# Performance work log

Measured on AMD Instinct MI355X. Metric: run time of the kernel, lower is better.

## Reference

```python
import jax, jax.numpy as jnp
import numpy as np

CHUNK = 32
HEADS = 4
EPS_RMS = 1e-5

def silu(x):
    return jax.nn.silu(x)

def l2norm(x, eps=1e-6):
    return x * jax.lax.rsqrt(jnp.sum(x * x, axis=-1, keepdims=True) + eps)

def short_conv(x, w):
    # x: (b, l, c); w: (c, K) depthwise causal conv, no bias
    K = w.shape[1]
    L = x.shape[1]
    xp = jnp.pad(x, ((0, 0), (K - 1, 0), (0, 0)))
    out = xp[:, 0:L, :] * w[:, 0]
    for k in range(1, K):
        out = out + xp[:, k:k + L, :] * w[:, k]
    return out

def delta_rule_chunkwise(q, k, v, beta, chunk=CHUNK):
    # q,k: (b,h,l,dk); v: (b,h,l,dv); beta: (b,h,l). l divisible by chunk.
    b, h, l, dk = q.shape
    dv = v.shape[-1]
    n = l // chunk
    q = l2norm(q)
    k = l2norm(k)
    v = v * beta[..., None]
    k_beta = k * beta[..., None]
    resh = lambda x: x.reshape(b, h, n, chunk, -1)
    q, k, v, k_beta = map(resh, (q, k, v, k_beta))
    strict_lower = jnp.tril(jnp.ones((chunk, chunk), bool), -1)
    # A = -(k_beta k^T) kept strictly lower triangular
    attn = jnp.where(strict_lower, -(k_beta @ jnp.swapaxes(k, -1, -2)), 0.0)
    # forward substitution: T = (I - A)^{-1} - I built row by row (fixed 32 rows)
    for i in range(1, chunk):
        row = attn[..., i, :]                                  # (b,h,n,c)
        new = attn[..., i, :i] + jnp.einsum('...j,...jk->...k', row, attn[..., :, :i])
        attn = attn.at[..., i, :i].set(new)
    attn = attn + jnp.eye(chunk, dtype=attn.dtype)
    u = attn @ v        # (b,h,n,c,dv)
    w = attn @ k_beta   # (b,h,n,c,dk)
    lower_incl = jnp.tril(jnp.ones((chunk, chunk), bool))
    qc, kc, uc, wc = [jnp.moveaxis(x, 2, 0) for x in (q, k, u, w)]
    S0 = jnp.zeros((b, h, dk, dv), q.dtype)
    def step(S, inp):
        q_i, k_i, u_i, w_i = inp
        attn_i = jnp.where(lower_incl, q_i @ jnp.swapaxes(k_i, -1, -2), 0.0)
        u_adj = u_i - w_i @ S
        o_i = q_i @ S + attn_i @ u_adj
        S = S + jnp.swapaxes(k_i, -1, -2) @ u_adj
        return S, o_i
    S, o = jax.lax.scan(step, S0, (qc, kc, uc, wc))
    o = jnp.moveaxis(o, 0, 2).reshape(b, h, l, dv)
    return o, S

def ema_rule(v, gamma):
    # v: (b,h,l,dv), gamma: (b,h,l); sequential EMA scan
    v_t = jnp.moveaxis(v, 2, 0)       # (l,b,h,dv)
    g_t = jnp.moveaxis(gamma, 2, 0)   # (l,b,h)
    s0 = jnp.zeros(v.shape[:2] + (v.shape[-1],), v.dtype)
    def step(s, inp):
        vt, gt = inp
        s = gt[..., None] * s + (1.0 - gt[..., None]) * vt
        return s, s
    s_fin, out = jax.lax.scan(step, s0, (v_t, g_t))
    return jnp.moveaxis(out, 0, 2), s_fin

def rms_norm(x, w, eps=EPS_RMS):
    return x * jax.lax.rsqrt(jnp.mean(x * x, axis=-1, keepdims=True) + eps) * w

def setup_inputs() -> dict:
    key = jax.random.key(0)
    ks = jax.random.split(key, 16)
    b, l, d = 4, 2048, 1024
    H, conv_K = HEADS, 4
    s = 0.02
    return {
        'hidden_states': jax.random.normal(ks[0], (b, l, d), jnp.float32),
        'Wq': jax.random.normal(ks[1], (d, d), jnp.float32) * s,
        'Wk': jax.random.normal(ks[2], (d, d), jnp.float32) * s,
        'Wv': jax.random.normal(ks[3], (d, d), jnp.float32) * s,
        'conv_q': jax.random.normal(ks[4], (d, conv_K), jnp.float32) * 0.3,
        'conv_k': jax.random.normal(ks[5], (d, conv_K), jnp.float32) * 0.3,
        'conv_v': jax.random.normal(ks[6], (d, conv_K), jnp.float32) * 0.3,
        'Wb': jax.random.normal(ks[7], (d, H), jnp.float32) * s,
        'Wdec': jax.random.normal(ks[8], (d, H), jnp.float32) * s,
        'Wmix': jax.random.normal(ks[9], (d, H), jnp.float32) * s,
        'conv_mix': jax.random.normal(ks[10], (H, conv_K), jnp.float32) * 0.3,
        'mix_bias': jnp.full((H,), -2.0, jnp.float32),
        'rms_w': jnp.ones((d // H,), jnp.float32),
        'Wo': jax.random.normal(ks[11], (d, d), jnp.float32) * s,
    }

def reference(hidden_states, Wq, Wk, Wv, conv_q, conv_k, conv_v, Wb, Wdec, Wmix, conv_mix, mix_bias, rms_w, Wo):
    b, l, d = hidden_states.shape
    H = HEADS
    dk = d // H
    dv = d // H
    # projections + causal depthwise short conv (silu activation inside conv)
    q = silu(short_conv(hidden_states @ Wq, conv_q))
    k = silu(short_conv(hidden_states @ Wk, conv_k))
    v = silu(short_conv(hidden_states @ Wv, conv_v))
    mix_inp = silu(short_conv(hidden_states @ Wmix, conv_mix))  # (b,l,H)
    # qk_activation == 'silu' applies an extra silu after conv (per source)
    q = silu(q)
    k = silu(k)
    # split heads -> (b,H,l,dh)
    to_heads = lambda x, dh: jnp.transpose(x.reshape(b, l, H, dh), (0, 2, 1, 3))
    q_d = to_heads(q, dk)
    k_d = to_heads(k, dk)
    v_d = to_heads(v, dv)
    beta = jax.nn.sigmoid(hidden_states @ Wb)           # (b,l,H)
    beta_d = jnp.transpose(beta, (0, 2, 1))             # (b,H,l)
    o_d, S = delta_rule_chunkwise(q_d, k_d, v_d, beta_d)
    o_d = jnp.transpose(o_d, (0, 2, 1, 3))              # (b,l,H,dv)
    # EMA branch
    gamma = jax.nn.sigmoid(hidden_states @ Wdec)        # (b,l,H)
    gamma_d = jnp.transpose(gamma, (0, 2, 1))
    ema_out, ema_state = ema_rule(v_d, gamma_d)
    ema_out = jnp.transpose(ema_out, (0, 2, 1, 3))      # (b,l,H,dv)
    # fine-grained head mix gate
    mix = jax.nn.sigmoid(mix_inp + mix_bias)            # (b,l,H)
    o = (1.0 - mix[..., None]) * o_d + mix[..., None] * ema_out
    # per-head RMSNorm then output projection
    o = rms_norm(o, rms_w)
    out = o.reshape(b, l, H * dv) @ Wo
    return out
```

## Files before the change

kernel.cpp:

```cpp
#include <hip/hip_runtime.h>
#include <hip/hip_bf16.h>

#define B 4
#define L 2048
#define D 1024
#define NH 4
#define DK 256
#define CHUNK 32
#define NCH 64
#define BH (B*NH)
#define ET 64
#define ENCH (L/ET)
#define TB 16

typedef __attribute__((ext_vector_type(8))) __bf16 bf16x8;
typedef __attribute__((ext_vector_type(4))) __bf16 bf16x4;
typedef __attribute__((ext_vector_type(4))) float f32x4;

__device__ inline unsigned short f2bf(float f) {
    union { float f; unsigned u; } v; v.f = f;
    unsigned r = v.u + 0x7fffu + ((v.u >> 16) & 1u);
    return (unsigned short)(r >> 16);
}
__device__ inline float bf2f(unsigned short h) {
    union { unsigned u; float f; } v; v.u = ((unsigned)h) << 16; return v.f;
}
__device__ inline float sigmoidf_(float x) { return 1.0f / (1.0f + __expf(-x)); }
__device__ inline float siluf_(float x) { return x / (1.0f + __expf(-x)); }

#define MFMA16(a, b, c) __builtin_amdgcn_mfma_f32_16x16x32_bf16((a), (b), (c), 0, 0, 0)

__device__ inline void bar_lds() {
    __builtin_amdgcn_s_waitcnt(0xC07F);
    __builtin_amdgcn_s_barrier();
}

__device__ inline void load_lds16(const unsigned short* g, unsigned short* l) {
    __builtin_amdgcn_global_load_lds(
        (const __attribute__((address_space(1))) unsigned int*)g,
        (__attribute__((address_space(3))) unsigned int*)l, 16, 0, 0);
}

__global__ __launch_bounds__(256) void k_wT(const float* Wq, const float* Wk, const float* Wv,
                                            const float* Wo, unsigned short* wT)
{
    __shared__ float tile[32][33];
    int z = blockIdx.z;
    const float* W = (z == 0) ? Wq : (z == 1) ? Wk : (z == 2) ? Wv : Wo;
    unsigned short* out = wT + (size_t)z * D * D;
    int kt = blockIdx.x * 32, nt = blockIdx.y * 32;
    int tx = threadIdx.x & 31, ty = threadIdx.x >> 5;
#pragma unroll
    for (int i = 0; i < 4; i++)
        tile[ty + 8 * i][tx] = W[(size_t)(kt + ty + 8 * i) * D + nt + tx];
    __syncthreads();
#pragma unroll
    for (int i = 0; i < 4; i++)
        out[(size_t)(nt + ty + 8 * i) * D + kt + tx] = f2bf(tile[tx][ty + 8 * i]);
}

__global__ __launch_bounds__(256) void k_cvt(const float* h, unsigned short* hb, int n4)
{
    int i = blockIdx.x * blockDim.x + threadIdx.x;
    int stride = gridDim.x * blockDim.x;
    const float4* h4 = (const float4*)h;
    for (; i < n4; i += stride) {
        float4 v = h4[i];
        ushort4 o;
        o.x = f2bf(v.x); o.y = f2bf(v.y); o.z = f2bf(v.z); o.w = f2bf(v.w);
        *(ushort4*)(hb + 4 * (size_t)i) = o;
    }
}

template<int NTOT, bool OUT_F32>
__global__ __launch_bounds__(256) void k_gemm_lds(const unsigned short* __restrict__ A,
                                                  const unsigned short* __restrict__ BT,
                                                  void* __restrict__ outp)
{
    __shared__ __align__(16) unsigned short As[128 * 32];
    __shared__ __align__(16) unsigned short Bs[128 * 32];
    const int K = 1024;
    int tid = threadIdx.x;
    int w = tid >> 6, lane = tid & 63;
    int r16 = lane & 15, quad = lane >> 4;
    int wm = w & 1, wn = w >> 1;
    int bm = blockIdx.x * 128;
    int bn = blockIdx.y * 128;
    int lrow = lane >> 2;
    int lcol = (lane & 3) * 8;
    f32x4 z4 = {0.f, 0.f, 0.f, 0.f};
    f32x4 acc[4][4];
#pragma unroll
    for (int i = 0; i < 4; i++)
#pragma unroll
        for (int j = 0; j < 4; j++) acc[i][j] = z4;

    for (int kt = 0; kt < K; kt += 32) {
#pragma unroll
        for (int j = 0; j < 2; j++) {
            int r0 = (w * 2 + j) * 16;
            load_lds16(A + (size_t)(bm + r0 + lrow) * K + kt + lcol, &As[r0 * 32]);
            load_lds16(BT + (size_t)(bn + r0 + lrow) * K + kt + lcol, &Bs[r0 * 32]);
        }
        __syncthreads();
        bf16x8 af[4], bf[4];
#pragma unroll
        for (int ms = 0; ms < 4; ms++)
            af[ms] = *(const bf16x8*)&As[(wm * 64 + ms * 16 + r16) * 32 + quad * 8];
#pragma unroll
        for (int ns = 0; ns < 4; ns++)
            bf[ns] = *(const bf16x8*)&Bs[(wn * 64 + ns * 16 + r16) * 32 + quad * 8];
#pragma unroll
        for (int ms = 0; ms < 4; ms++)
#pragma unroll
            for (int ns = 0; ns < 4; ns++)
                acc[ms][ns] = MFMA16(af[ms], bf[ns], acc[ms][ns]);
        __syncthreads();
    }
#pragma unroll
    for (int ms = 0; ms < 4; ms++)
#pragma unroll
        for (int ns = 0; ns < 4; ns++)
#pragma unroll
            for (int r = 0; r < 4; r++) {
                int m = bm + wm * 64 + ms * 16 + quad * 4 + r;
                int n = bn + wn * 64 + ns * 16 + r16;
                if (OUT_F32)
                    ((float*)outp)[(size_t)m * NTOT + n] = acc[ms][ns][r];
                else
                    ((unsigned short*)outp)[(size_t)m * NTOT + n] = f2bf(acc[ms][ns][r]);
            }
}

__global__ __launch_bounds__(256) void k_smallproj(const float* hid, const float* Wb, const float* Wd,
                                                   const float* Wm, float* beta, float* gamma, float* xmix)
{
    int wave = threadIdx.x >> 6, lane = threadIdx.x & 63;
    int row = blockIdx.x * 4 + wave;
    const float* hrow = hid + (size_t)row * D;
    float acc[12];
#pragma unroll
    for (int j = 0; j < 12; j++) acc[j] = 0.f;
    for (int i = 0; i < 16; i++) {
        int k = lane + 64 * i;
        float h = hrow[k];
        float4 wb = ((const float4*)Wb)[k];
        float4 wd = ((const float4*)Wd)[k];
        float4 wm = ((const float4*)Wm)[k];
        acc[0] += h * wb.x; acc[1] += h * wb.y; acc[2] += h * wb.z; acc[3] += h * wb.w;
        acc[4] += h * wd.x; acc[5] += h * wd.y; acc[6] += h * wd.z; acc[7] += h * wd.w;
        acc[8] += h * wm.x; acc[9] += h * wm.y; acc[10] += h * wm.z; acc[11] += h * wm.w;
    }
#pragma unroll
    for (int j = 0; j < 12; j++)
        for (int off = 32; off; off >>= 1) acc[j] += __shfl_xor(acc[j], off, 64);
    if (lane < 4) {
        beta[(size_t)row * 4 + lane] = sigmoidf_(acc[lane]);
        gamma[(size_t)row * 4 + lane] = sigmoidf_(acc[4 + lane]);
        xmix[(size_t)row * 4 + lane] = acc[8 + lane];
    }
}

__global__ __launch_bounds__(256) void k_convnorm(const unsigned short* __restrict__ xqkv,
                                                  const float* __restrict__ cq,
                                                  const float* __restrict__ ck,
                                                  const float* __restrict__ cv,
                                                  unsigned short* __restrict__ qn,
                                                  unsigned short* __restrict__ kn,
                                                  unsigned short* __restrict__ vb)
{
    int blk = blockIdx.x;
    int b = blk >> 7;
    int t0 = (blk & 127) * TB;
    int tid = threadIdx.x;
    int h = tid >> 6, lane = tid & 63;
    int c = tid * 4;

    float wq[4][4], wk[4][4], wv[4][4];
#pragma unroll
    for (int j = 0; j < 4; j++) {
        float4 a = *(const float4*)(cq + (size_t)(c + j) * 4);
        wq[j][0] = a.x; wq[j][1] = a.y; wq[j][2] = a.z; wq[j][3] = a.w;
        float4 d4 = *(const float4*)(ck + (size_t)(c + j) * 4);
        wk[j][0] = d4.x; wk[j][1] = d4.y; wk[j][2] = d4.z; wk[j][3] = d4.w;
        float4 e = *(const float4*)(cv + (size_t)(c + j) * 4);
        wv[j][0] = e.x; wv[j][1] = e.y; wv[j][2] = e.z; wv[j][3] = e.w;
    }

    float aq[4][4], ak[4][4], av[4][4];
#pragma unroll
    for (int s = 0; s < 4; s++)
#pragma unroll
        for (int j = 0; j < 4; j++) { aq[s][j] = 0.f; ak[s][j] = 0.f; av[s][j] = 0.f; }

    const unsigned short* xb = xqkv + (size_t)(b * L) * (3 * D) + c;

#pragma unroll
    for (int p = 0; p < 3; p++) {
        int r = t0 - 3 + p;
        if (r >= 0) {
            const unsigned short* pp = xb + (size_t)r * (3 * D);
            ushort4 xq = *(const ushort4*)pp;
            ushort4 xk = *(const ushort4*)(pp + D);
            ushort4 xv = *(const ushort4*)(pp + 2 * D);
            float fq[4] = {bf2f(xq.x), bf2f(xq.y), bf2f(xq.z), bf2f(xq.w)};
            float fk[4] = {bf2f(xk.x), bf2f(xk.y), bf2f(xk.z), bf2f(xk.w)};
            float fv[4] = {bf2f(xv.x), bf2f(xv.y), bf2f(xv.z), bf2f(xv.w)};
#pragma unroll
            for (int d = 3 - p; d <= 3; d++) {
                int s = (p + d + 1) & 3;
                int kk = 3 - d;
#pragma unroll
                for (int j = 0; j < 4; j++) {
                    aq[s][j] += wq[j][kk] * fq[j];
                    ak[s][j] += wk[j][kk] * fk[j];
                    av[s][j] += wv[j][kk] * fv[j];
                }
            }
        }
    }

    ushort4 sq2[2], sk2[2], sv2[2];
    {
        const unsigned short* pp = xb + (size_t)t0 * (3 * D);
        sq2[0] = *(const ushort4*)pp;
        sk2[0] = *(const ushort4*)(pp + D);
        sv2[0] = *(const ushort4*)(pp + 2 * D);
    }

#pragma unroll
    for (int i = 0; i < TB; i++) {
        if (i + 1 < TB) {
            const unsigned short* pp = xb + (size_t)(t0 + i + 1) * (3 * D);
            sq2[(i + 1) & 1] = *(const ushort4*)pp;
            sk2[(i + 1) & 1] = *(const ushort4*)(pp + D);
            sv2[(i + 1) & 1] = *(const ushort4*)(pp + 2 * D);
        }
        {
            ushort4 xq = sq2[i & 1], xk = sk2[i & 1], xv = sv2[i & 1];
            float fq[4] = {bf2f(xq.x), bf2f(xq.y), bf2f(xq.z), bf2f(xq.w)};
            float fk[4] = {bf2f(xk.x), bf2f(xk.y), bf2f(xk.z), bf2f(xk.w)};
            float fv[4] = {bf2f(xv.x), bf2f(xv.y), bf2f(xv.z), bf2f(xv.w)};
#pragma unroll
            for (int d = 0; d < 4; d++) {
                if (i + d < TB) {
                    int s = (i + d) & 3;
                    int kk = 3 - d;
#pragma unroll
                    for (int j = 0; j < 4; j++) {
                        aq[s][j] += wq[j][kk] * fq[j];
                        ak[s][j] += wk[j][kk] * fk[j];
                        av[s][j] += wv[j][kk] * fv[j];
                    }
                }
            }
        }
        {
            const int s = i & 3;
            float rq[4], rk[4], rv[4];
#pragma unroll
            for (int j = 0; j < 4; j++) {
                rq[j] = siluf_(siluf_(aq[s][j]));
                rk[j] = siluf_(siluf_(ak[s][j]));
                rv[j] = siluf_(av[s][j]);
            }
            float sqs = rq[0] * rq[0] + rq[1] * rq[1] + rq[2] * rq[2] + rq[3] * rq[3];
            float sks = rk[0] * rk[0] + rk[1] * rk[1] + rk[2] * rk[2] + rk[3] * rk[3];
            for (int off = 32; off; off >>= 1) {
                sqs += __shfl_xor(sqs, off, 64);
                sks += __shfl_xor(sks, off, 64);
            }
            float qs = rsqrtf(sqs + 1e-6f), ks = rsqrtf(sks + 1e-6f);
            int t = t0 + i;
            size_t oidx = ((size_t)(b * NH + h) * L + t) * DK + lane * 4;
            ushort4 oq, ok, ov;
            oq.x = f2bf(rq[0] * qs); oq.y = f2bf(rq[1] * qs); oq.z = f2bf(rq[2] * qs); oq.w = f2bf(rq[3] * qs);
            ok.x = f2bf(rk[0] * ks); ok.y = f2bf(rk[1] * ks); ok.z = f2bf(rk[2] * ks); ok.w = f2bf(rk[3] * ks);
            ov.x = f2bf(rv[0]); ov.y = f2bf(rv[1]); ov.z = f2bf(rv[2]); ov.w = f2bf(rv[3]);
            *(ushort4*)(qn + oidx) = oq;
            *(ushort4*)(kn + oidx) = ok;
            *(ushort4*)(vb + (size_t)(b * L + t) * D + c) = ov;
            if (i + 4 < TB) {
#pragma unroll
                for (int j = 0; j < 4; j++) { aq[s][j] = 0.f; ak[s][j] = 0.f; av[s][j] = 0.f; }
            }
        }
    }
}

__global__ __launch_bounds__(256) void k_convmix(const float* xmix, const float* cmix, float* mixinp)
{
    int idx = blockIdx.x * 256 + threadIdx.x;
    int h = idx & 3;
    int t = (idx >> 2) & (L - 1);
    int b = idx >> 13;
    float acc = 0.f;
#pragma unroll
    for (int kk = 0; kk < 4; kk++) {
        int tt = t - 3 + kk;
        if (tt >= 0) acc += cmix[h * 4 + kk] * xmix[((size_t)(b * L + tt) << 2) + h];
    }
    mixinp[idx] = siluf_(acc);
}

#define KTS 40
__global__ __launch_bounds__(256) void k_delta_pre(const unsigned short* qn, const unsigned short* kn,
                                                   const unsigned short* vb, const float* beta,
                                                   unsigned short* wneg, unsigned short* knT,
                                                   unsigned short* attnb, float* u)
{
    __shared__ __align__(16) unsigned short kTl[256 * KTS];
    __shared__ __align__(16) unsigned short vTl[256 * KTS];
    __shared__ __align__(16) unsigned short T2b[32 * KTS];
    __shared__ float Gs[32 * 33];
    int bx = blockIdx.x;
    int bh = bx >> 6, ch = bx & 63;
    int b = bh >> 2, h = bh & 3;
    int t0 = ch * 32;
    int tid = threadIdx.x;
    int w = tid >> 6, lane = tid & 63;
    int r16 = lane & 15, quad = lane >> 4;
    size_t rowbase = (size_t)(bh * L + t0);
    f32x4 z4 = {0.f, 0.f, 0.f, 0.f};

    if (w < 3) {
        int mi = (w == 0) ? 0 : 1;
        int ni = (w == 2) ? 1 : 0;
        const unsigned short* krm = kn + (rowbase + mi * 16 + r16) * DK;
        const unsigned short* krn = kn + (rowbase + ni * 16 + r16) * DK;
        const unsigned short* qrm = qn + (rowbase + mi * 16 + r16) * DK;
        f32x4 g = z4, qk = z4;
#pragma unroll
        for (int kt = 0; kt < 8; kt++) {
            bf16x8 a  = *(const bf16x8*)(krm + kt * 32 + quad * 8);
            bf16x8 bb = *(const bf16x8*)(krn + kt * 32 + quad * 8);
            bf16x8 qa = *(const bf16x8*)(qrm + kt * 32 + quad * 8);
            g  = MFMA16(a, bb, g);
            qk = MFMA16(qa, bb, qk);
        }
#pragma unroll
        for (int r = 0; r < 4; r++) {
            int i = mi * 16 + quad * 4 + r, j = ni * 16 + r16;
            Gs[i * 33 + j] = g[r];
            attnb[(size_t)(bh * 64 + ch) * 1024 + i * 32 + j] =
                (j <= i) ? f2bf(qk[r]) : (unsigned short)0;
        }
    } else {
#pragma unroll
        for (int r = 0; r < 4; r++) {
            int i = quad * 4 + r, j = 16 + r16;
            attnb[(size_t)(bh * 64 + ch) * 1024 + i * 32 + j] = 0;
        }
    }
    {
        int t = tid & 31, c0 = (tid >> 5) * 32;
        const unsigned short* krow = kn + (rowbase + t) * DK + c0;
        const unsigned short* vrow = vb + ((size_t)(b * L + t0 + t)) * D + h * DK + c0;
#pragma unroll
        for (int j = 0; j < 32; j += 4) {
            ushort4 kv = *(const ushort4*)(krow + j);
            ushort4 vv = *(const ushort4*)(vrow + j);
            kTl[(c0 + j + 0) * KTS + t] = kv.x;
            kTl[(c0 + j + 1) * KTS + t] = kv.y;
            kTl[(c0 + j + 2) * KTS + t] = kv.z;
            kTl[(c0 + j + 3) * KTS + t] = kv.w;
            vTl[(c0 + j + 0) * KTS + t] = vv.x;
            vTl[(c0 + j + 1) * KTS + t] = vv.y;
            vTl[(c0 + j + 2) * KTS + t] = vv.z;
            vTl[(c0 + j + 3) * KTS + t] = vv.w;
        }
    }
    __syncthreads();

    if (w == 0) {
        int c = lane & 31;
        float rr[32];
#pragma unroll
        for (int j = 0; j < 32; j++) rr[j] = Gs[j * 33 + c];
        rr[0] = 0.f;
        float bc = beta[(size_t)(b * L + t0 + c) * NH + h];
#pragma unroll
        for (int i = 1; i < 32; i++) {
            float bi = __shfl(bc, i, 64);
            float s = -bi * rr[i];
#pragma unroll
            for (int j = 1; j < i; j++) {
                float aij = -bi * __shfl(rr[i], j, 64);
                s += aij * ((c < j) ? rr[j] : 0.f);
            }
            rr[i] = (c < i) ? s : 0.f;
        }
        if (lane < 32) {
#pragma unroll
            for (int i = 0; i < 32; i++) {
                float val = (rr[i] + ((i == c) ? 1.f : 0.f)) * bc;
                T2b[i * KTS + c] = f2bf(val);
            }
        }
    } else {
        int idx = tid - 64;
        for (int rowc = idx; rowc < 256; rowc += 192) {
            unsigned short* kT = knT + ((size_t)(bh * 64 + ch) * DK + rowc) * 32;
#pragma unroll
            for (int seg = 0; seg < 4; seg++) {
                uint4 d = *(const uint4*)&kTl[rowc * KTS + seg * 8];
                *(uint4*)(kT + seg * 8) = d;
            }
        }
    }
    __syncthreads();

#pragma unroll
    for (int mt = 0; mt < 2; mt++) {
        bf16x8 ta = *(const bf16x8*)&T2b[(mt * 16 + r16) * KTS + quad * 8];
#pragma unroll
        for (int nt2 = 0; nt2 < 4; nt2++) {
            int nt = w * 4 + nt2;
            bf16x8 vb2 = *(const bf16x8*)&vTl[(nt * 16 + r16) * KTS + quad * 8];
            bf16x8 kb = *(const bf16x8*)&kTl[(nt * 16 + r16) * KTS + quad * 8];
            f32x4 uu = MFMA16(ta, vb2, z4);
            f32x4 ww = MFMA16(ta, kb, z4);
            float* ug = u + (rowbase + mt * 16 + quad * 4) * DK + nt * 16 + r16;
            unsigned short* wg = wneg + (rowbase + mt * 16 + quad * 4) * DK + nt * 16 + r16;
#pragma unroll
            for (int r = 0; r < 4; r++) {
                ug[(size_t)r * DK] = uu[r];
                wg[(size_t)r * DK] = f2bf(-ww[r]);
            }
        }
    }
}

__global__ __launch_bounds__(256) void k_ema_local(const unsigned short* v, const float* gamma,
                                                   float* ema_local, float* Acum,
                                                   float* s_end, float* Pchunk)
{
    __shared__ float gsh[ET];
    int blk = blockIdx.x;
    int bh = blk >> 5;
    int ch = blk & (ENCH - 1);
    int b = bh >> 2, h = bh & 3;
    int c = threadIdx.x;
    int t0 = ch * ET;
    if (c < ET) gsh[c] = gamma[(size_t)(b * L + t0 + c) * NH + h];
    __syncthreads();
    const unsigned short* vg = v + (size_t)(b * L + t0) * D + h * DK + c;
    float* eg = ema_local + (size_t)(b * L + t0) * D + h * DK + c;
    float* Ag = Acum + (size_t)bh * L + t0;
    float s = 0.f;
    float A = 1.f;
#pragma unroll 8
    for (int i = 0; i < ET; i++) {
        float g = gsh[i];
        s = g * s + (1.f - g) * bf2f(vg[(size_t)i * D]);
        A *= g;
        eg[(size_t)i * D] = s;
        if (c == 0) Ag[i] = A;
    }
    s_end[((size_t)bh * ENCH + ch) * DK + c] = s;
    if (c == 0) Pchunk[(size_t)bh * ENCH + ch] = A;
}

__global__ __launch_bounds__(256) void k_ema_carry(const float* s_end, const float* Pchunk, float* S_in)
{
    int bh = blockIdx.x;
    int c = threadIdx.x;
    float S = 0.f;
    for (int ch = 0; ch < ENCH; ch++) {
        S_in[((size_t)bh * ENCH + ch) * DK + c] = S;
        float P = Pchunk[(size_t)bh * ENCH + ch];
        S = P * S + s_end[((size_t)bh * ENCH + ch) * DK + c];
    }
}

#define STS 280
#define USTR 40
__global__ __launch_bounds__(128, 1) void k_scan(const unsigned short* qn, const unsigned short* wneg,
                                                 const unsigned short* knT, const unsigned short* attnb,
                                                 const float* u, float* od)
{
    __shared__ __align__(16) unsigned short st[16 * STS];
    __shared__ __align__(16) unsigned short uat[16 * USTR];
    int bh = blockIdx.x;
    int tile = blockIdx.y;
    int b = bh >> 2, h = bh & 3;
    int mo = threadIdx.x >> 6, lane = threadIdx.x & 63;
    int r16 = lane & 15, quad = lane >> 4;
    int cbase = tile * 16;
    f32x4 z4 = {0.f, 0.f, 0.f, 0.f};
    f32x4 sacc[8];
#pragma unroll
    for (int a = 0; a < 8; a++) sacc[a] = z4;
    const unsigned short* qb = qn + (size_t)bh * L * DK;
    const unsigned short* wb = wneg + (size_t)bh * L * DK;
    const float* ub = u + (size_t)bh * L * DK;
    const unsigned short* kTbase = knT + (size_t)bh * 64 * DK * 32;
    const unsigned short* atbase = attnb + (size_t)bh * 64 * 1024;
    int dkb = mo * 128;

    bf16x8 qf[2][8], wf[2][8];
    f32x4 au0[2];

    auto issue = [&](int ch, int par) {
        int t0 = ch * 32;
        const unsigned short* wrow = wb + (size_t)(t0 + 16 * mo + r16) * DK;
        const unsigned short* qrow = qb + (size_t)(t0 + 16 * mo + r16) * DK;
#pragma unroll
        for (int kt = 0; kt < 8; kt++) {
            qf[par][kt] = *(const bf16x8*)(qrow + kt * 32 + quad * 8);
            wf[par][kt] = *(const bf16x8*)(wrow + kt * 32 + quad * 8);
        }
        const float* up = ub + (size_t)(t0 + 16 * mo + quad * 4) * DK + cbase + r16;
        f32x4 a; a[0] = up[0]; a[1] = up[DK]; a[2] = up[2 * DK]; a[3] = up[3 * DK];
        au0[par] = a;
    };

    issue(0, 0);

    auto body = [&](int ch, int par) {
        int t0 = ch * 32;
        bf16x8 af = *(const bf16x8*)(atbase + (size_t)ch * 1024 + (16 * mo + r16) * 32 + quad * 8);
        const unsigned short* kTb = kTbase + (size_t)ch * DK * 32;
        bf16x8 kf[8];
#pragma unroll
        for (int a = 0; a < 8; a++)
            kf[a] = *(const bf16x8*)(kTb + (size_t)(dkb + a * 16 + r16) * 32 + quad * 8);

#pragma unroll
        for (int a = 0; a < 8; a++) {
            uint2 p;
            p.x = f2bf(sacc[a][0]) | ((unsigned)f2bf(sacc[a][1]) << 16);
            p.y = f2bf(sacc[a][2]) | ((unsigned)f2bf(sacc[a][3]) << 16);
            *(uint2*)&st[r16 * STS + dkb + a * 16 + quad * 4] = p;
        }
        if (ch + 1 < NCH) issue(ch + 1, par ^ 1);
        bar_lds();

        f32x4 au = au0[par], ao = z4;
#pragma unroll
        for (int kt = 0; kt < 8; kt++) {
            bf16x8 sfr = *(const bf16x8*)&st[r16 * STS + kt * 32 + quad * 8];
            au = MFMA16(wf[par][kt], sfr, au);
            ao = MFMA16(qf[par][kt], sfr, ao);
        }
        {
            uint2 p;
            p.x = f2bf(au[0]) | ((unsigned)f2bf(au[1]) << 16);
            p.y = f2bf(au[2]) | ((unsigned)f2bf(au[3]) << 16);
            *(uint2*)&uat[r16 * USTR + 16 * mo + quad * 4] = p;
        }
        bar_lds();

        {
            bf16x8 uf = *(const bf16x8*)&uat[r16 * USTR + quad * 8];
            ao = MFMA16(af, uf, ao);
            float* op = od + (size_t)(b * L + t0 + 16 * mo + quad * 4) * D + h * DK + cbase + r16;
            op[0] = ao[0]; op[D] = ao[1]; op[2 * D] = ao[2]; op[3 * D] = ao[3];
#pragma unroll
            for (int a = 0; a < 8; a++)
                sacc[a] = MFMA16(kf[a], uf, sacc[a]);
        }
    };

    for (int ch2 = 0; ch2 < NCH; ch2 += 2) {
        body(ch2, 0);
        body(ch2 + 1, 1);
    }
}

__global__ __launch_bounds__(256) void k_mixrms(const float* od, const float* ema_local,
                                                const float* Acum, const float* S_in,
                                                const float* mixinp,
                                                const float* mix_bias, const float* rms_w,
                                                unsigned short* onorm)
{
    int row = blockIdx.x;
    int tid = threadIdx.x;
    int h = tid >> 6, lane = tid & 63;
    int b = row >> 11, t = row & (L - 1);
    int bh = b * NH + h;
    int ch = t >> 6;
    float m = sigmoidf_(mixinp[(size_t)row * NH + h] + mix_bias[h]);
    int c = tid * 4;
    float A = Acum[(size_t)bh * L + t];
    float4 sin4 = *(const float4*)(S_in + ((size_t)bh * ENCH + ch) * DK + (c & (DK - 1)));
    float4 o = *(const float4*)(od + (size_t)row * D + c);
    float4 e = *(const float4*)(ema_local + (size_t)row * D + c);
    e.x += A * sin4.x; e.y += A * sin4.y; e.z += A * sin4.z; e.w += A * sin4.w;
    float x0 = o.x + m * (e.x - o.x);
    float x1 = o.y + m * (e.y - o.y);
    float x2 = o.z + m * (e.z - o.z);
    float x3 = o.w + m * (e.w - o.w);
    float ss = x0 * x0 + x1 * x1 + x2 * x2 + x3 * x3;
    for (int off = 32; off; off >>= 1) ss += __shfl_xor(ss, off, 64);
    float scale = rsqrtf(ss * (1.0f / 256.0f) + 1e-5f);
    float4 w = *(const float4*)(rms_w + lane * 4);
    uint2 p;
    p.x = f2bf(x0 * scale * w.x) | ((unsigned)f2bf(x1 * scale * w.y) << 16);
    p.y = f2bf(x2 * scale * w.z) | ((unsigned)f2bf(x3 * scale * w.w) << 16);
    *(uint2*)(onorm + (size_t)row * D + c) = p;
}

extern "C" void kernel_launch(void* const* d_in, const int* in_sizes, int n_in,
                              void* d_out, int out_size, void* d_ws, size_t ws_size,
                              hipStream_t stream)
{
    (void)in_sizes; (void)n_in; (void)out_size; (void)ws_size;
    const float* hidden   = (const float*)d_in[0];
    const float* Wq       = (const float*)d_in[1];
    const float* Wk       = (const float*)d_in[2];
    const float* Wv       = (const float*)d_in[3];
    const float* conv_q   = (const float*)d_in[4];
    const float* conv_k   = (const float*)d_in[5];
    const float* conv_v   = (const float*)d_in[6];
    const float* Wb       = (const float*)d_in[7];
    const float* Wdec     = (const float*)d_in[8];
    const float* Wmix     = (const float*)d_in[9];
    const float* conv_mix = (const float*)d_in[10];
    const float* mix_bias = (const float*)d_in[11];
    const float* rms_w    = (const float*)d_in[12];
    const float* Wo       = (const float*)d_in[13];
    float* out = (float*)d_out;

    char* ws = (char*)d_ws;
    size_t off = 0;
    auto alloc = [&](size_t bytes) -> char* {
        char* p = ws + off;
        off += (bytes + 255) & ~(size_t)255;
        return p;
    };
    unsigned short* wT    = (unsigned short*)alloc((size_t)4 * D * D * 2);
    unsigned short* hidB  = (unsigned short*)alloc((size_t)B * L * D * 2);
    unsigned short* xqkv  = (unsigned short*)alloc((size_t)B * L * 3 * D * 2);
    float* beta   = (float*)alloc((size_t)B * L * NH * 4);
    float* gamma  = (float*)alloc((size_t)B * L * NH * 4);
    float* xmix   = (float*)alloc((size_t)B * L * NH * 4);
    float* mixinp = (float*)alloc((size_t)B * L * NH * 4);
    float* qbuf   = (float*)alloc((size_t)B * L * D * 4);
    float* kbuf   = (float*)alloc((size_t)B * L * D * 4);
    unsigned short* vb = (unsigned short*)alloc((size_t)B * L * D * 2);
    float* u      = (float*)alloc((size_t)B * L * D * 4);
    unsigned short* attnb = (unsigned short*)alloc((size_t)BH * NCH * CHUNK * CHUNK * 2);
    unsigned short* onorm = (unsigned short*)alloc((size_t)B * L * D * 2);
    unsigned short* kn    = (unsigned short*)alloc((size_t)B * L * D * 2);
    unsigned short* qn    = (unsigned short*)alloc((size_t)B * L * D * 2);
    float* Acum   = (float*)alloc((size_t)BH * L * 4);
    float* s_end  = (float*)alloc((size_t)BH * ENCH * DK * 4);
    float* Pchunk = (float*)alloc((size_t)BH * ENCH * 4);
    float* S_in   = (float*)alloc((size_t)BH * ENCH * DK * 4);

    unsigned short* wneg = xqkv + (size_t)B * L * D;
    unsigned short* knT  = xqkv + (size_t)2 * B * L * D;
    float* ema_local = qbuf;
    float* od  = kbuf;

    k_wT<<<dim3(32, 32, 4), 256, 0, stream>>>(Wq, Wk, Wv, Wo, wT);
    k_cvt<<<dim3(2048), 256, 0, stream>>>(hidden, hidB, B * L * D / 4);
    k_gemm_lds<3 * D, false><<<dim3(64, 24), 256, 0, stream>>>(hidB, wT, xqkv);
    k_smallproj<<<dim3(B * L / 4), 256, 0, stream>>>(hidden, Wb, Wdec, Wmix, beta, gamma, xmix);
    k_convnorm<<<dim3(B * L / TB), 256, 0, stream>>>(xqkv, conv_q, conv_k, conv_v, qn, kn, vb);
    k_convmix<<<dim3(B * L * NH / 256), 256, 0, stream>>>(xmix, conv_mix, mixinp);
    k_delta_pre<<<dim3(BH * NCH), 256, 0, stream>>>(qn, kn, vb, beta, wneg, knT, attnb, u);
    k_ema_local<<<dim3(BH * ENCH), 256, 0, stream>>>(vb, gamma, ema_local, Acum, s_end, Pchunk);
    k_ema_carry<<<dim3(BH), 256, 0, stream>>>(s_end, Pchunk, S_in);
    k_scan<<<dim3(16, 16), 128, 0, stream>>>(qn, wneg, knT, attnb, u, od);
    k_mixrms<<<dim3(B * L), 256, 0, stream>>>(od, ema_local, Acum, S_in, mixinp, mix_bias, rms_w, onorm);
    k_gemm_lds<D, true><<<dim3(64, 8), 256, 0, stream>>>(onorm, wT + (size_t)3 * D * D, out);
}
```

Baseline: 459.5 us.

## Fuse bf16 conversion into smallproj, remap GEMM tiles per XCD, store intermediates as bf16

Removes the separate hidden-state conversion kernel by having k_smallproj write the bf16 copy while it reads the row, saving one full read of the input. The GEMM block index is remapped so that groups of M-tiles sharing a B column land on the same XCD, which is meant to improve L2 reuse. The delta-rule output and the EMA local output are now stored as bf16 instead of fp32, halving their write and read traffic into the mix/RMS kernel at some cost in precision.

```diff
diff --git a/kernel.cpp b/kernel.cpp
--- a/kernel.cpp
+++ b/kernel.cpp
@@ -59,19 +59,6 @@
         out[(size_t)(nt + ty + 8 * i) * D + kt + tx] = f2bf(tile[tx][ty + 8 * i]);
 }
 
-__global__ __launch_bounds__(256) void k_cvt(const float* h, unsigned short* hb, int n4)
-{
-    int i = blockIdx.x * blockDim.x + threadIdx.x;
-    int stride = gridDim.x * blockDim.x;
-    const float4* h4 = (const float4*)h;
-    for (; i < n4; i += stride) {
-        float4 v = h4[i];
-        ushort4 o;
-        o.x = f2bf(v.x); o.y = f2bf(v.y); o.z = f2bf(v.z); o.w = f2bf(v.w);
-        *(ushort4*)(hb + 4 * (size_t)i) = o;
-    }
-}
-
 template<int NTOT, bool OUT_F32>
 __global__ __launch_bounds__(256) void k_gemm_lds(const unsigned short* __restrict__ A,
                                                   const unsigned short* __restrict__ BT,
@@ -84,8 +71,10 @@
     int w = tid >> 6, lane = tid & 63;
     int r16 = lane & 15, quad = lane >> 4;
     int wm = w & 1, wn = w >> 1;
-    int bm = blockIdx.x * 128;
-    int bn = blockIdx.y * 128;
+    int lin = blockIdx.x + gridDim.x * blockIdx.y;
+    int xcd = lin & 7, tt = lin >> 3;
+    int bm = (xcd * 8 + (tt & 7)) * 128;
+    int bn = (tt >> 3) * 128;
     int lrow = lane >> 2;
     int lcol = (lane & 3) * 8;
     f32x4 z4 = {0.f, 0.f, 0.f, 0.f};
@@ -133,17 +122,20 @@
 }
 
 __global__ __launch_bounds__(256) void k_smallproj(const float* hid, const float* Wb, const float* Wd,
-                                                   const float* Wm, float* beta, float* gamma, float* xmix)
+                                                   const float* Wm, float* beta, float* gamma, float* xmix,
+                                                   unsigned short* hb)
 {
     int wave = threadIdx.x >> 6, lane = threadIdx.x & 63;
     int row = blockIdx.x * 4 + wave;
     const float* hrow = hid + (size_t)row * D;
+    unsigned short* hbrow = hb + (size_t)row * D;
     float acc[12];
 #pragma unroll
     for (int j = 0; j < 12; j++) acc[j] = 0.f;
     for (int i = 0; i < 16; i++) {
         int k = lane + 64 * i;
         float h = hrow[k];
+        hbrow[k] = f2bf(h);
         float4 wb = ((const float4*)Wb)[k];
         float4 wd = ((const float4*)Wd)[k];
         float4 wm = ((const float4*)Wm)[k];
@@ -432,7 +424,7 @@
 }
 
 __global__ __launch_bounds__(256) void k_ema_local(const unsigned short* v, const float* gamma,
-                                                   float* ema_local, float* Acum,
+                                                   unsigned short* ema_local, float* Acum,
                                                    float* s_end, float* Pchunk)
 {
     __shared__ float gsh[ET];
@@ -445,7 +437,7 @@
     if (c < ET) gsh[c] = gamma[(size_t)(b * L + t0 + c) * NH + h];
     __syncthreads();
     const unsigned short* vg = v + (size_t)(b * L + t0) * D + h * DK + c;
-    float* eg = ema_local + (size_t)(b * L + t0) * D + h * DK + c;
+    unsigned short* eg = ema_local + (size_t)(b * L + t0) * D + h * DK + c;
     float* Ag = Acum + (size_t)bh * L + t0;
     float s = 0.f;
     float A = 1.f;
@@ -454,7 +446,7 @@
         float g = gsh[i];
         s = g * s + (1.f - g) * bf2f(vg[(size_t)i * D]);
         A *= g;
-        eg[(size_t)i * D] = s;
+        eg[(size_t)i * D] = f2bf(s);
         if (c == 0) Ag[i] = A;
     }
     s_end[((size_t)bh * ENCH + ch) * DK + c] = s;
@@ -477,7 +469,7 @@
 #define USTR 40
 __global__ __launch_bounds__(128, 1) void k_scan(const unsigned short* qn, const unsigned short* wneg,
                                                  const unsigned short* knT, const unsigned short* attnb,
-                                                 const float* u, float* od)
+                                                 const float* u, unsigned short* od)
 {
     __shared__ __align__(16) unsigned short st[16 * STS];
     __shared__ __align__(16) unsigned short uat[16 * USTR];
@@ -554,8 +546,9 @@
         {
             bf16x8 uf = *(const bf16x8*)&uat[r16 * USTR + quad * 8];
             ao = MFMA16(af, uf, ao);
-            float* op = od + (size_t)(b * L + t0 + 16 * mo + quad * 4) * D + h * DK + cbase + r16;
-            op[0] = ao[0]; op[D] = ao[1]; op[2 * D] = ao[2]; op[3 * D] = ao[3];
+            unsigned short* op = od + (size_t)(b * L + t0 + 16 * mo + quad * 4) * D + h * DK + cbase + r16;
+            op[0] = f2bf(ao[0]); op[D] = f2bf(ao[1]);
+            op[2 * D] = f2bf(ao[2]); op[3 * D] = f2bf(ao[3]);
 #pragma unroll
             for (int a = 0; a < 8; a++)
                 sacc[a] = MFMA16(kf[a], uf, sacc[a]);
@@ -568,7 +561,7 @@
     }
 }
 
-__global__ __launch_bounds__(256) void k_mixrms(const float* od, const float* ema_local,
+__global__ __launch_bounds__(256) void k_mixrms(const unsigned short* od, const unsigned short* ema_local,
                                                 const float* Acum, const float* S_in,
                                                 const float* mixinp,
                                                 const float* mix_bias, const float* rms_w,
@@ -584,13 +577,17 @@
     int c = tid * 4;
     float A = Acum[(size_t)bh * L + t];
     float4 sin4 = *(const float4*)(S_in + ((size_t)bh * ENCH + ch) * DK + (c & (DK - 1)));
-    float4 o = *(const float4*)(od + (size_t)row * D + c);
-    float4 e = *(const float4*)(ema_local + (size_t)row * D + c);
-    e.x += A * sin4.x; e.y += A * sin4.y; e.z += A * sin4.z; e.w += A * sin4.w;
-    float x0 = o.x + m * (e.x - o.x);
-    float x1 = o.y + m * (e.y - o.y);
-    float x2 = o.z + m * (e.z - o.z);
-    float x3 = o.w + m * (e.w - o.w);
+    ushort4 o4 = *(const ushort4*)(od + (size_t)row * D + c);
+    ushort4 e4 = *(const ushort4*)(ema_local + (size_t)row * D + c);
+    float ox = bf2f(o4.x), oy = bf2f(o4.y), oz = bf2f(o4.z), ow = bf2f(o4.w);
+    float ex = bf2f(e4.x) + A * sin4.x;
+    float ey = bf2f(e4.y) + A * sin4.y;
+    float ez = bf2f(e4.z) + A * sin4.z;
+    float ew = bf2f(e4.w) + A * sin4.w;
+    float x0 = ox + m * (ex - ox);
+    float x1 = oy + m * (ey - oy);
+    float x2 = oz + m * (ez - oz);
+    float x3 = ow + m * (ew - ow);
     float ss = x0 * x0 + x1 * x1 + x2 * x2 + x3 * x3;
     for (int off = 32; off; off >>= 1) ss += __shfl_xor(ss, off, 64);
     float scale = rsqrtf(ss * (1.0f / 256.0f) + 1e-5f);
@@ -651,13 +648,12 @@
 
     unsigned short* wneg = xqkv + (size_t)B * L * D;
     unsigned short* knT  = xqkv + (size_t)2 * B * L * D;
-    float* ema_local = qbuf;
-    float* od  = kbuf;
+    unsigned short* ema_local = (unsigned short*)qbuf;
+    unsigned short* od  = (unsigned short*)kbuf;
 
     k_wT<<<dim3(32, 32, 4), 256, 0, stream>>>(Wq, Wk, Wv, Wo, wT);
-    k_cvt<<<dim3(2048), 256, 0, stream>>>(hidden, hidB, B * L * D / 4);
+    k_smallproj<<<dim3(B * L / 4), 256, 0, stream>>>(hidden, Wb, Wdec, Wmix, beta, gamma, xmix, hidB);
     k_gemm_lds<3 * D, false><<<dim3(64, 24), 256, 0, stream>>>(hidB, wT, xqkv);
-    k_smallproj<<<dim3(B * L / 4), 256, 0, stream>>>(hidden, Wb, Wdec, Wmix, beta, gamma, xmix);
     k_convnorm<<<dim3(B * L / TB), 256, 0, stream>>>(xqkv, conv_q, conv_k, conv_v, qn, kn, vb);
     k_convmix<<<dim3(B * L * NH / 256), 256, 0, stream>>>(xmix, conv_mix, mixinp);
     k_delta_pre<<<dim3(BH * NCH), 256, 0, stream>>>(qn, kn, vb, beta, wneg, knT, attnb, u);
```

Measured after the change: 451.3 us. No clear change (-1.8%).
